# Performance work log

Measured on AMD Instinct MI355X. Metric: run time of the kernel, lower is better.

## Reference

```python
import jax, jax.numpy as jnp
import numpy as np

MARGIN = 0.3
EPS = 1e-6  # torch pairwise_distance eps (added to the difference before norm)


def _sample_triplets(labels, B):
    """Vectorized equivalent of the per-row nonzero()+randint() mining loop.

    pos_idx[i] ~ Uniform{j : labels[j] == labels[i]}   (always non-empty: i itself)
    neg_idx[i] ~ Uniform{j : labels[j] != labels[i]}, fallback Uniform[0,B) if empty.
    Uniform-noise argmax over the masked set == uniform random choice.
    """
    key = jax.random.key(42)
    k1, k2, k3 = jax.random.split(key, 3)
    eq = labels[:, None] == labels[None, :]              # [B, B]
    pos_idx = jnp.argmax(jnp.where(eq, jax.random.uniform(k1, (B, B)), -1.0), axis=1)
    neg_scores = jnp.where(~eq, jax.random.uniform(k2, (B, B)), -1.0)
    has_neg = jnp.any(~eq, axis=1)
    neg_idx = jnp.where(has_neg,
                        jnp.argmax(neg_scores, axis=1),
                        jax.random.randint(k3, (B,), 0, B))
    return pos_idx, neg_idx


def _pdist(X, A, D):
    """out[i, j] = || A[j] - X[i] + EPS ||_2  (torch pairwise_distance semantics),
    computed via gram matrices instead of a [B,B,D] intermediate:
    ||a - x + eps||^2 = ||a||^2 + ||x||^2 - 2 a.x + 2*eps*(sum a - sum x) + D*eps^2.
    """
    sq = (jnp.sum(A * A, axis=1)[None, :]
          + jnp.sum(X * X, axis=1)[:, None]
          - 2.0 * (X @ A.T)
          + 2.0 * EPS * (jnp.sum(A, axis=1)[None, :] - jnp.sum(X, axis=1)[:, None])
          + D * EPS * EPS)
    return jnp.sqrt(jnp.maximum(sq, 1e-12))


def setup_inputs() -> dict:
    key = jax.random.key(0)
    kf, kl = jax.random.split(key)
    B, D, NUM_IDS = 4096, 1024, 512
    features = jax.random.normal(kf, (B, D), dtype=jnp.float32)
    labels = jax.random.randint(kl, (B,), 0, NUM_IDS, dtype=jnp.int32)
    return {"features": features, "labels": labels}


def reference(features, labels):
    B, D = features.shape
    pos_idx, neg_idx = _sample_triplets(labels, B)
    P = features[pos_idx]   # positives, [B, D]
    N = features[neg_idx]   # negatives, [B, D]
    # Original torch code stacks positives/negatives as [B,1,D] vs anchors [B,D],
    # so TripletMarginLoss broadcasts to ALL-PAIRS [B,B] distances:
    # dap[i, j] = ||anchor_j - positive_i + eps||, same for dan.
    dap = _pdist(P, features, D)  # [B, B]
    dan = _pdist(N, features, D)  # [B, B]
    return jnp.mean(jax.nn.relu(dap - dan + MARGIN))
```

## Files before the change

kernel.cpp:

```cpp
#include <hip/hip_runtime.h>
#include <stdint.h>

#define BSZ 4096
#define DIM 1024
#define EPSV 1e-6f
#define MARGINV 0.3f
#define LROWS 8

#define TF_ROT(x0, x1, r) { x0 += x1; x1 = ((x1 << r) | (x1 >> (32 - r))); x1 ^= x0; }

__host__ __device__ __forceinline__ void threefry2x32(uint32_t k0, uint32_t k1,
                                                      uint32_t c0, uint32_t c1,
                                                      uint32_t& o0, uint32_t& o1) {
  uint32_t ks2 = k0 ^ k1 ^ 0x1BD11BDAu;
  uint32_t x0 = c0 + k0;
  uint32_t x1 = c1 + k1;
  TF_ROT(x0, x1, 13) TF_ROT(x0, x1, 15) TF_ROT(x0, x1, 26) TF_ROT(x0, x1, 6)
  x0 += k1;  x1 += ks2 + 1u;
  TF_ROT(x0, x1, 17) TF_ROT(x0, x1, 29) TF_ROT(x0, x1, 16) TF_ROT(x0, x1, 24)
  x0 += ks2; x1 += k0 + 2u;
  TF_ROT(x0, x1, 13) TF_ROT(x0, x1, 15) TF_ROT(x0, x1, 26) TF_ROT(x0, x1, 6)
  x0 += k0;  x1 += k1 + 3u;
  TF_ROT(x0, x1, 17) TF_ROT(x0, x1, 29) TF_ROT(x0, x1, 16) TF_ROT(x0, x1, 24)
  x0 += k1;  x1 += ks2 + 4u;
  TF_ROT(x0, x1, 13) TF_ROT(x0, x1, 15) TF_ROT(x0, x1, 26) TF_ROT(x0, x1, 6)
  x0 += ks2; x1 += k0 + 5u;
  o0 = x0; o1 = x1;
}

__device__ __forceinline__ uint16_t f2bf(float f) {
  uint32_t u = __float_as_uint(f);
  u += 0x7FFFu + ((u >> 16) & 1u);
  return (uint16_t)(u >> 16);
}

__global__ __launch_bounds__(256) void prep_kernel(const float* __restrict__ F,
                                                   uint8_t* __restrict__ Fq,
                                                   float* __restrict__ norm2,
                                                   float* __restrict__ sums,
                                                   float* __restrict__ nv,
                                                   float* __restrict__ acc,
                                                   unsigned int* __restrict__ ticket) {
  const int w = threadIdx.x >> 6, l = threadIdx.x & 63;
  const int r = blockIdx.x * 4 + w;
  const float4* src = (const float4*)(F + (size_t)r * DIM);
  uint32_t* dst = (uint32_t*)(Fq + (size_t)r * DIM);
  float s = 0.f, q = 0.f;
#pragma unroll
  for (int c = 0; c < 4; ++c) {
    float4 v = src[c * 64 + l];
    s += (v.x + v.y) + (v.z + v.w);
    q += v.x * v.x + v.y * v.y + v.z * v.z + v.w * v.w;
    int wd = 0;
    wd = __builtin_amdgcn_cvt_pk_fp8_f32(v.x, v.y, wd, false);
    wd = __builtin_amdgcn_cvt_pk_fp8_f32(v.z, v.w, wd, true);
    dst[c * 64 + l] = (uint32_t)wd;
  }
  for (int off = 32; off; off >>= 1) { s += __shfl_xor(s, off); q += __shfl_xor(q, off); }
  if (l == 0) {
    norm2[r] = q; sums[r] = s;
    nv[r] = q + 2.0f * EPSV * s;
  }
  if (blockIdx.x == 0 && threadIdx.x == 0) { acc[0] = 0.f; ticket[0] = 0u; }
}

__global__ __launch_bounds__(256) void sample_kernel(const int* __restrict__ labels,
                                                     int* __restrict__ pos_idx,
                                                     int* __restrict__ neg_idx,
                                                     uint32_t p0, uint32_t p1,
                                                     uint32_t n0, uint32_t n1) {
  __shared__ int plist[64];
  __shared__ int pcnt;
  __shared__ unsigned long long swp;
  __shared__ unsigned long long swn[4];
  const int i = blockIdx.x, t = threadIdx.x;
  if (t == 0) { pcnt = 0; swp = 0ull; }
  int lj[16];
#pragma unroll
  for (int c = 0; c < 16; ++c) lj[c] = labels[c * 256 + t];
  const int li = labels[i];
  __syncthreads();
  const uint32_t base = (uint32_t)i * (uint32_t)BSZ + (uint32_t)t;
  uint32_t bestn = 0u;
#pragma unroll
  for (int c = 0; c < 16; ++c) {
    uint32_t y0, y1;
    threefry2x32(n0, n1, 0u, base + (uint32_t)(c * 256), y0, y1);
    const uint32_t pack = (((y0 ^ y1) >> 9) << 4) | (uint32_t)(15 - c);
    const bool eq = (lj[c] == li);
    if (eq) {
      int sl = atomicAdd(&pcnt, 1);
      if (sl < 64) plist[sl] = c * 256 + t;
    }
    const uint32_t v = eq ? 0u : pack;
    if (v > bestn) bestn = v;
  }
  unsigned long long keyn = 0ull;
  if (bestn) {
    const int c = 15 - (int)(bestn & 15u);
    const int j = c * 256 + t;
    keyn = ((unsigned long long)(bestn >> 4) << 32) | (uint32_t)(~j);
  }
  for (int off = 32; off; off >>= 1) {
    unsigned long long o = __shfl_xor(keyn, off);
    if (o > keyn) keyn = o;
  }
  const int w = t >> 6, lane = t & 63;
  if (lane == 0) swn[w] = keyn;
  __syncthreads();
  const int cnt = pcnt < 64 ? pcnt : 64;
  if (t < cnt) {
    const int j = plist[t];
    uint32_t y0, y1;
    threefry2x32(p0, p1, 0u, (uint32_t)i * (uint32_t)BSZ + (uint32_t)j, y0, y1);
    const unsigned long long key =
        ((unsigned long long)((y0 ^ y1) >> 9) << 32) | (uint32_t)(~j);
    atomicMax(&swp, key);
  }
  __syncthreads();
  if (t == 0) {
    unsigned long long vn = swn[0];
#pragma unroll
    for (int qd = 1; qd < 4; ++qd) if (swn[qd] > vn) vn = swn[qd];
    neg_idx[i] = (vn == 0ull) ? 0 : (int)(~(uint32_t)vn);
    pos_idx[i] = (int)(~(uint32_t)swp);
  }
}

using int8v = __attribute__((ext_vector_type(8))) int;
using int4v = __attribute__((ext_vector_type(4))) int;
using f32x4 = __attribute__((ext_vector_type(4))) float;

__device__ __forceinline__ void async_load16(const void* g, void* l) {
  __builtin_amdgcn_global_load_lds((__attribute__((address_space(1))) void*)g,
                                   (__attribute__((address_space(3))) void*)l, 16, 0, 0);
}

__global__ __launch_bounds__(256) void gemm_kernel(const uint8_t* __restrict__ Fq,
                                                   uint16_t* __restrict__ Gb) {
  const int p = blockIdx.x;
  int by = (int)((sqrtf(8.0f * (float)p + 1.0f) - 1.0f) * 0.5f);
  if ((by + 1) * (by + 2) / 2 <= p) ++by;
  if (by * (by + 1) / 2 > p) --by;
  const int bx = p - by * (by + 1) / 2;

  __shared__ __align__(16) uint8_t lA[128 * 128];
  __shared__ __align__(16) uint8_t lB[128 * 128];
  const int t = threadIdx.x;
  const int l = t & 63;
  const int w = t >> 6;
  const int wm = (w >> 1) * 64;
  const int wn = (w & 1) * 64;
  const int bm = bx * 128;
  const int bn = by * 128;

  f32x4 acc[4][4] = {};

  const int srow = t >> 3;
  const int scol = (((t & 7) ^ ((t >> 3) & 7)) << 4);
  const uint8_t* gA0 = Fq + (size_t)(bm + srow) * DIM + scol;
  const uint8_t* gB0 = Fq + (size_t)(bn + srow) * DIM + scol;

  const int fr = l & 15;
  const int c0 = (l >> 4) * 2;
  int offA[4][2], offB[4][2];
#pragma unroll
  for (int tm = 0; tm < 4; ++tm) {
    const int fra = wm + tm * 16 + fr, sw = fra & 7;
    offA[tm][0] = fra * 128 + ((c0 ^ sw) << 4);
    offA[tm][1] = fra * 128 + (((c0 + 1) ^ sw) << 4);
    const int frb = wn + tm * 16 + fr, sb = frb & 7;
    offB[tm][0] = frb * 128 + ((c0 ^ sb) << 4);
    offB[tm][1] = frb * 128 + (((c0 + 1) ^ sb) << 4);
  }

  for (int it = 0; it < 8; ++it) {
    const int k0 = it * 128;
    __syncthreads();
#pragma unroll
    for (int ld = 0; ld < 4; ++ld) {
      async_load16(gA0 + (size_t)ld * 32 * DIM + k0, (char*)lA + (ld * 256 + t) * 16);
      async_load16(gB0 + (size_t)ld * 32 * DIM + k0, (char*)lB + (ld * 256 + t) * 16);
    }
    __syncthreads();
    int8v av[4], bv[4];
#pragma unroll
    for (int tm = 0; tm < 4; ++tm) {
      int4v alo = *(const int4v*)&lA[offA[tm][0]];
      int4v ahi = *(const int4v*)&lA[offA[tm][1]];
      av[tm] = __builtin_shufflevector(alo, ahi, 0, 1, 2, 3, 4, 5, 6, 7);
      int4v blo = *(const int4v*)&lB[offB[tm][0]];
      int4v bhi = *(const int4v*)&lB[offB[tm][1]];
      bv[tm] = __builtin_shufflevector(blo, bhi, 0, 1, 2, 3, 4, 5, 6, 7);
    }
#pragma unroll
    for (int tm = 0; tm < 4; ++tm)
#pragma unroll
      for (int tn = 0; tn < 4; ++tn)
        acc[tm][tn] = __builtin_amdgcn_mfma_scale_f32_16x16x128_f8f6f4(
            av[tm], bv[tn], acc[tm][tn],
            0, 0,
            0, 0x7F7F7F7F,
            0, 0x7F7F7F7F);
  }
  const int cr = (l >> 4) * 4;
  const int cc = l & 15;
#pragma unroll
  for (int tm = 0; tm < 4; ++tm)
#pragma unroll
    for (int tn = 0; tn < 4; ++tn) {
      const int row0 = bm + wm + tm * 16 + cr;
      const int col  = bn + wn + tn * 16 + cc;
      ushort h0 = f2bf(acc[tm][tn][0]), h1 = f2bf(acc[tm][tn][1]);
      ushort h2 = f2bf(acc[tm][tn][2]), h3 = f2bf(acc[tm][tn][3]);
      Gb[(size_t)(row0 + 0) * BSZ + col] = h0;
      Gb[(size_t)(row0 + 1) * BSZ + col] = h1;
      Gb[(size_t)(row0 + 2) * BSZ + col] = h2;
      Gb[(size_t)(row0 + 3) * BSZ + col] = h3;
      ushort4 v = make_ushort4(h0, h1, h2, h3);
      *(ushort4*)&Gb[(size_t)col * BSZ + row0] = v;
    }
}

__device__ __forceinline__ float bfl(uint32_t w) { return __uint_as_float(w << 16); }
__device__ __forceinline__ float bfh(uint32_t w) { return __uint_as_float(w & 0xFFFF0000u); }

__global__ __launch_bounds__(256) void loss_kernel(const uint16_t* __restrict__ Gb,
                                                   const float* __restrict__ norm2,
                                                   const float* __restrict__ sums,
                                                   const float* __restrict__ nv,
                                                   const int* __restrict__ pos_idx,
                                                   const int* __restrict__ neg_idx,
                                                   float* __restrict__ acc,
                                                   unsigned int* __restrict__ ticket,
                                                   float* __restrict__ out) {
  const int i0 = blockIdx.x * LROWS, t = threadIdx.x;
  const float deps2 = (float)DIM * EPSV * EPSV;
  float ca[LROWS], cb[LROWS];
  const uint4* Ga[LROWS];
  const uint4* Gn[LROWS];
#pragma unroll
  for (int r = 0; r < LROWS; ++r) {
    const int a = pos_idx[i0 + r], b = neg_idx[i0 + r];
    ca[r] = norm2[a] - 2.0f * EPSV * sums[a] + deps2;
    cb[r] = norm2[b] - 2.0f * EPSV * sums[b] + deps2;
    Ga[r] = (const uint4*)(Gb + (size_t)a * BSZ);
    Gn[r] = (const uint4*)(Gb + (size_t)b * BSZ);
  }
  const float4* N4 = (const float4*)nv;
  float s = 0.f;
#pragma unroll
  for (int c = 0; c < 2; ++c) {
    const int q = c * 256 + t;
    const float4 nva = N4[q * 2];
    const float4 nvb = N4[q * 2 + 1];
    float nj[8] = {nva.x, nva.y, nva.z, nva.w, nvb.x, nvb.y, nvb.z, nvb.w};
#pragma unroll
    for (int r = 0; r < LROWS; ++r) {
      const uint4 ga = Ga[r][q], gn = Gn[r][q];
      const float capr = ca[r], cbpr = cb[r];
      float gav[8] = {bfl(ga.x), bfh(ga.x), bfl(ga.y), bfh(ga.y),
                      bfl(ga.z), bfh(ga.z), bfl(ga.w), bfh(ga.w)};
      float gnv[8] = {bfl(gn.x), bfh(gn.x), bfl(gn.y), bfh(gn.y),
                      bfl(gn.z), bfh(gn.z), bfl(gn.w), bfh(gn.w)};
#pragma unroll
      for (int e = 0; e < 8; ++e) {
        const float dap = sqrtf(fmaxf(fmaf(-2.f, gav[e], nj[e] + capr), 1e-12f));
        const float dan = sqrtf(fmaxf(fmaf(-2.f, gnv[e], nj[e] + cbpr), 1e-12f));
        s += fmaxf(dap - dan + MARGINV, 0.f);
      }
    }
  }
  for (int off = 32; off; off >>= 1) s += __shfl_xor(s, off);
  __shared__ float ps[4];
  const int w = t >> 6, lane = t & 63;
  if (lane == 0) ps[w] = s;
  __syncthreads();
  if (t == 0) {
    atomicAdd(acc, (ps[0] + ps[1]) + (ps[2] + ps[3]));
    __threadfence();
    unsigned int old = __hip_atomic_fetch_add(ticket, 1u, __ATOMIC_ACQ_REL,
                                              __HIP_MEMORY_SCOPE_AGENT);
    if (old == (unsigned int)(gridDim.x - 1)) {
      float total = __hip_atomic_load(acc, __ATOMIC_ACQUIRE, __HIP_MEMORY_SCOPE_AGENT);
      out[0] = total * (1.0f / ((float)BSZ * (float)BSZ));
    }
  }
}

extern "C" void kernel_launch(void* const* d_in, const int* in_sizes, int n_in,
                              void* d_out, int out_size, void* d_ws, size_t ws_size,
                              hipStream_t stream) {
  const float* feat = (const float*)d_in[0];
  const int* labels = (const int*)d_in[1];
  float* out = (float*)d_out;

  char* ws = (char*)d_ws;
  uint16_t* Gb     = (uint16_t*)ws;
  uint8_t* Fq      = (uint8_t*)(ws + (size_t)33554432);
  float* norm2     = (float*)(ws + (size_t)37748736);
  float* sums      = (float*)(ws + (size_t)37748736 + 16384);
  float* nv        = (float*)(ws + (size_t)37748736 + 32768);
  int* pos_idx     = (int*)  (ws + (size_t)37748736 + 49152);
  int* neg_idx     = (int*)  (ws + (size_t)37748736 + 65536);
  float* acc       = (float*)(ws + (size_t)37748736 + 81920);
  unsigned int* tk = (unsigned int*)(ws + (size_t)37748736 + 81924);

  uint32_t k1a, k1b, k2a, k2b;
  threefry2x32(0u, 42u, 0u, 0u, k1a, k1b);
  threefry2x32(0u, 42u, 0u, 1u, k2a, k2b);

  prep_kernel<<<dim3(BSZ / 4), dim3(256), 0, stream>>>(feat, Fq, norm2, sums, nv, acc, tk);
  sample_kernel<<<dim3(BSZ), dim3(256), 0, stream>>>(labels, pos_idx, neg_idx, k1a, k1b, k2a, k2b);
  gemm_kernel<<<dim3(528), dim3(256), 0, stream>>>(Fq, Gb);
  loss_kernel<<<dim3(BSZ / LROWS), dim3(256), 0, stream>>>(Gb, norm2, sums, nv, pos_idx,
                                                           neg_idx, acc, tk, out);
}
```

Measured before the change: 168.9 us.

## Rebalance sampling and loss kernels; replace float atomic accumulation with per-block partials

The sampling kernel now handles four anchor rows per block, reusing the label loads held in registers across those rows and folding per-wave maxima into shared memory with atomicMax. The loss kernel goes back to one row per block, issuing all global loads up front, and writes a per-block partial sum instead of doing a global float atomicAdd. The last block to finish reduces all partials, which makes the sum deterministic and removes contention on a single atomic. The trade-off is more, smaller loss blocks and fewer sampling blocks, plus a serial final reduction in the last block.

New measurement: 328.7 us. 94.6% more time.

```diff
diff --git a/kernel.cpp b/kernel.cpp
--- a/kernel.cpp
+++ b/kernel.cpp
@@ -5,7 +5,7 @@
 #define DIM 1024
 #define EPSV 1e-6f
 #define MARGINV 0.3f
-#define LROWS 8
+#define SROWS 4
 
 #define TF_ROT(x0, x1, r) { x0 += x1; x1 = ((x1 << r) | (x1 >> (32 - r))); x1 ^= x0; }
 
@@ -39,7 +39,6 @@
                                                    float* __restrict__ norm2,
                                                    float* __restrict__ sums,
                                                    float* __restrict__ nv,
-                                                   float* __restrict__ acc,
                                                    unsigned int* __restrict__ ticket) {
   const int w = threadIdx.x >> 6, l = threadIdx.x & 63;
   const int r = blockIdx.x * 4 + w;
@@ -61,7 +60,7 @@
     norm2[r] = q; sums[r] = s;
     nv[r] = q + 2.0f * EPSV * s;
   }
-  if (blockIdx.x == 0 && threadIdx.x == 0) { acc[0] = 0.f; ticket[0] = 0u; }
+  if (blockIdx.x == 0 && threadIdx.x == 0) ticket[0] = 0u;
 }
 
 __global__ __launch_bounds__(256) void sample_kernel(const int* __restrict__ labels,
@@ -69,61 +68,65 @@
                                                      int* __restrict__ neg_idx,
                                                      uint32_t p0, uint32_t p1,
                                                      uint32_t n0, uint32_t n1) {
-  __shared__ int plist[64];
-  __shared__ int pcnt;
-  __shared__ unsigned long long swp;
-  __shared__ unsigned long long swn[4];
-  const int i = blockIdx.x, t = threadIdx.x;
-  if (t == 0) { pcnt = 0; swp = 0ull; }
+  __shared__ int plist[SROWS][64];
+  __shared__ int pcnt[SROWS];
+  __shared__ unsigned long long swp[SROWS];
+  __shared__ unsigned long long swn[SROWS];
+  const int t = threadIdx.x;
+  const int i0 = blockIdx.x * SROWS;
+  if (t < SROWS) { pcnt[t] = 0; swp[t] = 0ull; swn[t] = 0ull; }
   int lj[16];
 #pragma unroll
   for (int c = 0; c < 16; ++c) lj[c] = labels[c * 256 + t];
-  const int li = labels[i];
-  __syncthreads();
-  const uint32_t base = (uint32_t)i * (uint32_t)BSZ + (uint32_t)t;
-  uint32_t bestn = 0u;
-#pragma unroll
-  for (int c = 0; c < 16; ++c) {
-    uint32_t y0, y1;
-    threefry2x32(n0, n1, 0u, base + (uint32_t)(c * 256), y0, y1);
-    const uint32_t pack = (((y0 ^ y1) >> 9) << 4) | (uint32_t)(15 - c);
-    const bool eq = (lj[c] == li);
-    if (eq) {
-      int sl = atomicAdd(&pcnt, 1);
-      if (sl < 64) plist[sl] = c * 256 + t;
-    }
-    const uint32_t v = eq ? 0u : pack;
-    if (v > bestn) bestn = v;
-  }
-  unsigned long long keyn = 0ull;
-  if (bestn) {
-    const int c = 15 - (int)(bestn & 15u);
-    const int j = c * 256 + t;
-    keyn = ((unsigned long long)(bestn >> 4) << 32) | (uint32_t)(~j);
-  }
-  for (int off = 32; off; off >>= 1) {
-    unsigned long long o = __shfl_xor(keyn, off);
-    if (o > keyn) keyn = o;
-  }
-  const int w = t >> 6, lane = t & 63;
-  if (lane == 0) swn[w] = keyn;
-  __syncthreads();
-  const int cnt = pcnt < 64 ? pcnt : 64;
-  if (t < cnt) {
-    const int j = plist[t];
-    uint32_t y0, y1;
-    threefry2x32(p0, p1, 0u, (uint32_t)i * (uint32_t)BSZ + (uint32_t)j, y0, y1);
-    const unsigned long long key =
-        ((unsigned long long)((y0 ^ y1) >> 9) << 32) | (uint32_t)(~j);
-    atomicMax(&swp, key);
-  }
-  __syncthreads();
-  if (t == 0) {
-    unsigned long long vn = swn[0];
-#pragma unroll
-    for (int qd = 1; qd < 4; ++qd) if (swn[qd] > vn) vn = swn[qd];
-    neg_idx[i] = (vn == 0ull) ? 0 : (int)(~(uint32_t)vn);
-    pos_idx[i] = (int)(~(uint32_t)swp);
+  __syncthreads();
+  const int lane = t & 63;
+  for (int r = 0; r < SROWS; ++r) {
+    const int li = labels[i0 + r];
+    const uint32_t base = (uint32_t)(i0 + r) * (uint32_t)BSZ + (uint32_t)t;
+    uint32_t bestn = 0u;
+#pragma unroll
+    for (int c = 0; c < 16; ++c) {
+      uint32_t y0, y1;
+      threefry2x32(n0, n1, 0u, base + (uint32_t)(c * 256), y0, y1);
+      const uint32_t pack = (((y0 ^ y1) >> 9) << 4) | (uint32_t)(15 - c);
+      const bool eq = (lj[c] == li);
+      if (eq) {
+        int sl = atomicAdd(&pcnt[r], 1);
+        if (sl < 64) plist[r][sl] = c * 256 + t;
+      }
+      const uint32_t v = eq ? 0u : pack;
+      if (v > bestn) bestn = v;
+    }
+    unsigned long long keyn = 0ull;
+    if (bestn) {
+      const int c = 15 - (int)(bestn & 15u);
+      const int j = c * 256 + t;
+      keyn = ((unsigned long long)(bestn >> 4) << 32) | (uint32_t)(~j);
+    }
+    for (int off = 32; off; off >>= 1) {
+      unsigned long long o = __shfl_xor(keyn, off);
+      if (o > keyn) keyn = o;
+    }
+    if (lane == 0) atomicMax(&swn[r], keyn);
+  }
+  __syncthreads();
+  const int w = t >> 6;
+  {
+    const int cnt = pcnt[w] < 64 ? pcnt[w] : 64;
+    if (lane < cnt) {
+      const int j = plist[w][lane];
+      uint32_t y0, y1;
+      threefry2x32(p0, p1, 0u, (uint32_t)(i0 + w) * (uint32_t)BSZ + (uint32_t)j, y0, y1);
+      const unsigned long long key =
+          ((unsigned long long)((y0 ^ y1) >> 9) << 32) | (uint32_t)(~j);
+      atomicMax(&swp[w], key);
+    }
+  }
+  __syncthreads();
+  if (t < SROWS) {
+    pos_idx[i0 + t] = (int)(~(uint32_t)swp[t]);
+    const unsigned long long vn = swn[t];
+    neg_idx[i0 + t] = (vn == 0ull) ? 0 : (int)(~(uint32_t)vn);
   }
 }
 
@@ -231,60 +234,63 @@
                                                    const float* __restrict__ nv,
                                                    const int* __restrict__ pos_idx,
                                                    const int* __restrict__ neg_idx,
-                                                   float* __restrict__ acc,
+                                                   float* __restrict__ partial,
                                                    unsigned int* __restrict__ ticket,
                                                    float* __restrict__ out) {
-  const int i0 = blockIdx.x * LROWS, t = threadIdx.x;
+  const int i = blockIdx.x, t = threadIdx.x;
+  const int a = pos_idx[i], b = neg_idx[i];
   const float deps2 = (float)DIM * EPSV * EPSV;
-  float ca[LROWS], cb[LROWS];
-  const uint4* Ga[LROWS];
-  const uint4* Gn[LROWS];
-#pragma unroll
-  for (int r = 0; r < LROWS; ++r) {
-    const int a = pos_idx[i0 + r], b = neg_idx[i0 + r];
-    ca[r] = norm2[a] - 2.0f * EPSV * sums[a] + deps2;
-    cb[r] = norm2[b] - 2.0f * EPSV * sums[b] + deps2;
-    Ga[r] = (const uint4*)(Gb + (size_t)a * BSZ);
-    Gn[r] = (const uint4*)(Gb + (size_t)b * BSZ);
-  }
+  const float ca = norm2[a] - 2.0f * EPSV * sums[a] + deps2;
+  const float cb = norm2[b] - 2.0f * EPSV * sums[b] + deps2;
+  const uint4* Ga = (const uint4*)(Gb + (size_t)a * BSZ);
+  const uint4* Gn = (const uint4*)(Gb + (size_t)b * BSZ);
   const float4* N4 = (const float4*)nv;
+  uint4 ga[2], gn[2];
+  float4 njv[4];
+  ga[0] = Ga[t * 2]; ga[1] = Ga[t * 2 + 1];
+  gn[0] = Gn[t * 2]; gn[1] = Gn[t * 2 + 1];
+#pragma unroll
+  for (int k = 0; k < 4; ++k) njv[k] = N4[t * 4 + k];
   float s = 0.f;
 #pragma unroll
-  for (int c = 0; c < 2; ++c) {
-    const int q = c * 256 + t;
-    const float4 nva = N4[q * 2];
-    const float4 nvb = N4[q * 2 + 1];
-    float nj[8] = {nva.x, nva.y, nva.z, nva.w, nvb.x, nvb.y, nvb.z, nvb.w};
-#pragma unroll
-    for (int r = 0; r < LROWS; ++r) {
-      const uint4 ga = Ga[r][q], gn = Gn[r][q];
-      const float capr = ca[r], cbpr = cb[r];
-      float gav[8] = {bfl(ga.x), bfh(ga.x), bfl(ga.y), bfh(ga.y),
-                      bfl(ga.z), bfh(ga.z), bfl(ga.w), bfh(ga.w)};
-      float gnv[8] = {bfl(gn.x), bfh(gn.x), bfl(gn.y), bfh(gn.y),
-                      bfl(gn.z), bfh(gn.z), bfl(gn.w), bfh(gn.w)};
-#pragma unroll
-      for (int e = 0; e < 8; ++e) {
-        const float dap = sqrtf(fmaxf(fmaf(-2.f, gav[e], nj[e] + capr), 1e-12f));
-        const float dan = sqrtf(fmaxf(fmaf(-2.f, gnv[e], nj[e] + cbpr), 1e-12f));
-        s += fmaxf(dap - dan + MARGINV, 0.f);
-      }
+  for (int h = 0; h < 2; ++h) {
+    const uint4 gau = ga[h], gnu = gn[h];
+    float gav[8] = {bfl(gau.x), bfh(gau.x), bfl(gau.y), bfh(gau.y),
+                    bfl(gau.z), bfh(gau.z), bfl(gau.w), bfh(gau.w)};
+    float gnv[8] = {bfl(gnu.x), bfh(gnu.x), bfl(gnu.y), bfh(gnu.y),
+                    bfl(gnu.z), bfh(gnu.z), bfl(gnu.w), bfh(gnu.w)};
+    const float4 na = njv[h * 2], nb = njv[h * 2 + 1];
+    float nj[8] = {na.x, na.y, na.z, na.w, nb.x, nb.y, nb.z, nb.w};
+#pragma unroll
+    for (int e = 0; e < 8; ++e) {
+      const float dap = sqrtf(fmaxf(fmaf(-2.f, gav[e], nj[e] + ca), 1e-12f));
+      const float dan = sqrtf(fmaxf(fmaf(-2.f, gnv[e], nj[e] + cb), 1e-12f));
+      s += fmaxf(dap - dan + MARGINV, 0.f);
     }
   }
   for (int off = 32; off; off >>= 1) s += __shfl_xor(s, off);
   __shared__ float ps[4];
+  __shared__ bool amLast;
   const int w = t >> 6, lane = t & 63;
   if (lane == 0) ps[w] = s;
   __syncthreads();
   if (t == 0) {
-    atomicAdd(acc, (ps[0] + ps[1]) + (ps[2] + ps[3]));
+    partial[i] = (ps[0] + ps[1]) + (ps[2] + ps[3]);
     __threadfence();
     unsigned int old = __hip_atomic_fetch_add(ticket, 1u, __ATOMIC_ACQ_REL,
                                               __HIP_MEMORY_SCOPE_AGENT);
-    if (old == (unsigned int)(gridDim.x - 1)) {
-      float total = __hip_atomic_load(acc, __ATOMIC_ACQUIRE, __HIP_MEMORY_SCOPE_AGENT);
-      out[0] = total * (1.0f / ((float)BSZ * (float)BSZ));
-    }
+    amLast = (old == (unsigned int)(gridDim.x - 1));
+  }
+  __syncthreads();
+  if (amLast) {
+    float v = 0.f;
+    for (int k = t; k < BSZ; k += 256)
+      v += __hip_atomic_load(&partial[k], __ATOMIC_RELAXED, __HIP_MEMORY_SCOPE_AGENT);
+    for (int off = 32; off; off >>= 1) v += __shfl_xor(v, off);
+    if (lane == 0) ps[w] = v;
+    __syncthreads();
+    if (t == 0)
+      out[0] = ((ps[0] + ps[1]) + (ps[2] + ps[3])) * (1.0f / ((float)BSZ * (float)BSZ));
   }
 }
 
@@ -303,16 +309,17 @@
   float* nv        = (float*)(ws + (size_t)37748736 + 32768);
   int* pos_idx     = (int*)  (ws + (size_t)37748736 + 49152);
   int* neg_idx     = (int*)  (ws + (size_t)37748736 + 65536);
-  float* acc       = (float*)(ws + (size_t)37748736 + 81920);
-  unsigned int* tk = (unsigned int*)(ws + (size_t)37748736 + 81924);
+  float* partial   = (float*)(ws + (size_t)37748736 + 81920);
+  unsigned int* tk = (unsigned int*)(ws + (size_t)37748736 + 98304);
 
   uint32_t k1a, k1b, k2a, k2b;
   threefry2x32(0u, 42u, 0u, 0u, k1a, k1b);
   threefry2x32(0u, 42u, 0u, 1u, k2a, k2b);
 
-  prep_kernel<<<dim3(BSZ / 4), dim3(256), 0, stream>>>(feat, Fq, norm2, sums, nv, acc, tk);
-  sample_kernel<<<dim3(BSZ), dim3(256), 0, stream>>>(labels, pos_idx, neg_idx, k1a, k1b, k2a, k2b);
+  prep_kernel<<<dim3(BSZ / 4), dim3(256), 0, stream>>>(feat, Fq, norm2, sums, nv, tk);
+  sample_kernel<<<dim3(BSZ / SROWS), dim3(256), 0, stream>>>(labels, pos_idx, neg_idx,
+                                                             k1a, k1b, k2a, k2b);
   gemm_kernel<<<dim3(528), dim3(256), 0, stream>>>(Fq, Gb);
-  loss_kernel<<<dim3(BSZ / LROWS), dim3(256), 0, stream>>>(Gb, norm2, sums, nv, pos_idx,
-                                                           neg_idx, acc, tk, out);
-}
+  loss_kernel<<<dim3(BSZ), dim3(256), 0, stream>>>(Gb, norm2, sums, nv, pos_idx,
+                                                   neg_idx, partial, tk, out);
+}
```
